# Optimization experiments

Measured on AMD Instinct MI355X. Metric: run time of the kernel, lower is better.

## Reference

```python
import jax, jax.numpy as jnp
import numpy as np

N_NODES = 100000
N_EDGES = 1600000
H = 64
TEM = 30.0
LN_EPS = 1e-5


def _mk_params(key):
    ks = jax.random.split(key, 6)
    s = 0.05
    p = {
        # edge_mlp: Linear(2H,H) relu Linear(H,H) relu (act_last=True)
        'We1': jax.random.normal(ks[0], (2 * H, H), jnp.float32) * s,
        'be1': jnp.zeros((H,), jnp.float32),
        'We2': jax.random.normal(ks[1], (H, H), jnp.float32) * s,
        'be2': jnp.zeros((H,), jnp.float32),
        # edge_inf: Linear(H,1)
        'Winf': jax.random.normal(ks[2], (H, 1), jnp.float32) * s,
        'binf': jnp.zeros((1,), jnp.float32),
        # node_mlp: Linear(2H,H) relu Linear(H,H) (no act_last)
        'Wn1': jax.random.normal(ks[3], (2 * H, H), jnp.float32) * s,
        'bn1': jnp.zeros((H,), jnp.float32),
        'Wn2': jax.random.normal(ks[4], (H, H), jnp.float32) * s,
        'bn2': jnp.zeros((H,), jnp.float32),
        # LayerNorm(H)
        'ln_g': jnp.ones((H,), jnp.float32),
        'ln_b': jnp.zeros((H,), jnp.float32),
    }
    return p


def setup_inputs() -> dict:
    key = jax.random.key(0)
    k1, k2, k3, k4 = jax.random.split(key, 4)
    inp = {
        'h': jax.random.normal(k1, (N_NODES, H), jnp.float32),
        'x': jax.random.normal(k2, (N_NODES, 3), jnp.float32),
        'edge_index': jax.random.randint(k3, (2, N_EDGES), 0, N_NODES, jnp.int64),
    }
    inp.update(_mk_params(k4))
    return inp


def _layernorm(z, g, b):
    mu = jnp.mean(z, axis=-1, keepdims=True)
    var = jnp.var(z, axis=-1, keepdims=True)
    return (z - mu) * jax.lax.rsqrt(var + LN_EPS) * g + b


def reference(h, x, edge_index, We1, be1, We2, be2, Winf, binf, Wn1, bn1, Wn2, bn2, ln_g, ln_b):
    src = edge_index[0]
    dst = edge_index[1]
    hi = h[dst]                      # [E, H]
    hj = h[src]                      # [E, H]
    rel_x = x[dst] - x[src]          # [E, 3]
    d_sq = jnp.sum(rel_x ** 2, axis=-1, keepdims=True)  # [E, 1]

    # edge MLP (relu, act_last=True)
    e_in = jnp.concatenate([hi, hj], axis=-1)           # [E, 2H]
    mij = jax.nn.relu(e_in @ We1 + be1)
    mij = jax.nn.relu(mij @ We2 + be2)                  # [E, H]

    eij = mij @ Winf + binf                             # [E, 1]
    edge_dis = jax.nn.sigmoid(TEM / (jnp.sqrt(d_sq) + 1e-8))
    edge_weights = jax.nn.sigmoid(eij * edge_dis)       # [E, 1]

    mi = jax.ops.segment_sum(mij * edge_weights, dst, num_segments=h.shape[0])  # [N, H]

    n_in = jnp.concatenate([mi, h], axis=-1)            # [N, 2H]
    upd = jax.nn.relu(n_in @ Wn1 + bn1) @ Wn2 + bn2     # [N, H] (no act_last)

    h_out = _layernorm(h + upd, ln_g, ln_b)
    return (h_out, x)
```

## Files before the change

### kernel.cpp

```cpp
#include <hip/hip_runtime.h>
#include <hip/hip_bf16.h>
#include <hip/hip_fp16.h>
#include <math.h>

#define HDIM 64
#define NN   100000
#define NE   1600000
#define TEMP 30.0f
#define LNEPS 1e-5f

#define GSH   6
#define GSZ   64
#define NB    1563
#define NBLK  64
#define EPB   (NE / NBLK)
#define NCNT  (NB * NBLK)
#define SCANB2 98
#define FSTR  72

typedef __attribute__((ext_vector_type(8))) short bf16x8;
typedef __attribute__((ext_vector_type(4))) float f32x4;
typedef _Float16 __attribute__((ext_vector_type(2))) h2t;

__device__ __forceinline__ short f2bf(float f) {
    __hip_bfloat16 b = __float2bfloat16(f);
    short s; __builtin_memcpy(&s, &b, 2); return s;
}
__device__ __forceinline__ unsigned pk2(float lo, float hi) {
    return (unsigned)(unsigned short)f2bf(lo) | ((unsigned)(unsigned short)f2bf(hi) << 16);
}
__device__ __forceinline__ short f2h(float f) {
    __half h = __float2half(f);
    short s; __builtin_memcpy(&s, &h, 2); return s;
}
__device__ __forceinline__ unsigned pk2h(float lo, float hi) {
    return (unsigned)(unsigned short)f2h(lo) | ((unsigned)(unsigned short)f2h(hi) << 16);
}
__device__ __forceinline__ unsigned pk_add_relu(unsigned a, unsigned b) {
    h2t x, y;
    __builtin_memcpy(&x, &a, 4); __builtin_memcpy(&y, &b, 4);
    h2t r = x + y;
    unsigned u; __builtin_memcpy(&u, &r, 4);
    const unsigned msk = ((u & 0x80008000u) >> 15) * 0xFFFFu;
    return u & ~msk;
}
__device__ __forceinline__ float sigmoidf_(float z) { return 1.0f / (1.0f + __expf(-z)); }

extern "C" __global__ void __launch_bounds__(256, 2)
front_kernel(const float* __restrict__ h,
             const float* __restrict__ We1, const float* __restrict__ be1,
             unsigned short* __restrict__ Pt, unsigned short* __restrict__ Pb,
             const int* __restrict__ ei, int* __restrict__ cnt3)
{
    __shared__ float fx[4][1024];
    const int b = blockIdx.x;

    if (b < NBLK) {
        int* hbin = (int*)&fx[0][0];
        const int tid = threadIdx.x;
        for (int k = tid; k < NB; k += 256) hbin[k] = 0;
        __syncthreads();
        const int i0 = b * EPB;
        for (int i = i0 + tid; i < i0 + EPB; i += 256)
            atomicAdd(&hbin[ei[NE + i] >> GSH], 1);
        __syncthreads();
        for (int k = tid; k < NB; k += 256)
            cnt3[k * NBLK + b] = hbin[k];
        return;
    }

    const int pb   = b - NBLK;
    const int tid  = threadIdx.x;
    const int wib  = tid >> 6;
    const int lane = tid & 63;
    const int e = lane & 15, g = lane >> 4;
    float* fb = &fx[wib][0];
    const int se = ((e & 1) << 4) | ((e >> 1) & 3);

    bf16x8 At[4][2], Ab[4][2];
    f32x4 b1r[4];
    #pragma unroll
    for (int t = 0; t < 4; ++t) {
        #pragma unroll
        for (int ks = 0; ks < 2; ++ks) {
            bf16x8 a, bb;
            #pragma unroll
            for (int j = 0; j < 8; ++j) {
                a[j]  = f2bf(We1[(32 * ks + 8 * g + j) * 64 + 16 * t + e]);
                bb[j] = f2bf(We1[(64 + 32 * ks + 8 * g + j) * 64 + 16 * t + e]);
            }
            At[t][ks] = a; Ab[t][ks] = bb;
        }
        #pragma unroll
        for (int r = 0; r < 4; ++r) b1r[t][r] = be1[16 * t + 4 * g + r];
    }

    const int gwid = pb * 4 + wib;
    const int nw   = 512 * 4;

    for (int tile = gwid; tile < NN / 16; tile += nw) {
        const int node = tile * 16 + e;

        bf16x8 B[2];
        #pragma unroll
        for (int ks = 0; ks < 2; ++ks) {
            const float4* p = (const float4*)(h + (size_t)node * 64 + ks * 32 + 8 * g);
            const float4 f0 = p[0], f1 = p[1];
            bf16x8 bb;
            bb[0] = f2bf(f0.x); bb[1] = f2bf(f0.y); bb[2] = f2bf(f0.z); bb[3] = f2bf(f0.w);
            bb[4] = f2bf(f1.x); bb[5] = f2bf(f1.y); bb[6] = f2bf(f1.z); bb[7] = f2bf(f1.w);
            B[ks] = bb;
        }

        f32x4 aT[4], aB[4];
        #pragma unroll
        for (int t = 0; t < 4; ++t) {
            aT[t] = b1r[t];
            aB[t] = (f32x4){0.f, 0.f, 0.f, 0.f};
            #pragma unroll
            for (int ks = 0; ks < 2; ++ks) {
                aT[t] = __builtin_amdgcn_mfma_f32_16x16x32_bf16(At[t][ks], B[ks], aT[t], 0, 0, 0);
                aB[t] = __builtin_amdgcn_mfma_f32_16x16x32_bf16(Ab[t][ks], B[ks], aB[t], 0, 0, 0);
            }
        }

        #pragma unroll
        for (int t = 0; t < 4; ++t)
            #pragma unroll
            for (int r = 0; r < 4; ++r)
                fb[e * 64 + ((16 * t + 4 * g + r) ^ se)] = aT[t][r];
        #pragma unroll
        for (int q = 0; q < 2; ++q) {
            const int row = q * 8 + (lane >> 3);
            const int sr  = ((row & 1) << 4) | ((row >> 1) & 3);
            const int c0  = (lane & 7) * 8;
            uint4 o;
            o.x = pk2h(fb[row * 64 + ((c0 + 0) ^ sr)], fb[row * 64 + ((c0 + 1) ^ sr)]);
            o.y = pk2h(fb[row * 64 + ((c0 + 2) ^ sr)], fb[row * 64 + ((c0 + 3) ^ sr)]);
            o.z = pk2h(fb[row * 64 + ((c0 + 4) ^ sr)], fb[row * 64 + ((c0 + 5) ^ sr)]);
            o.w = pk2h(fb[row * 64 + ((c0 + 6) ^ sr)], fb[row * 64 + ((c0 + 7) ^ sr)]);
            *(uint4*)((char*)Pt + (size_t)tile * 2048 + q * 1024 + lane * 16) = o;
        }

        #pragma unroll
        for (int t = 0; t < 4; ++t)
            #pragma unroll
            for (int r = 0; r < 4; ++r)
                fb[e * 64 + ((16 * t + 4 * g + r) ^ se)] = aB[t][r];
        #pragma unroll
        for (int q = 0; q < 2; ++q) {
            const int row = q * 8 + (lane >> 3);
            const int sr  = ((row & 1) << 4) | ((row >> 1) & 3);
            const int c0  = (lane & 7) * 8;
            uint4 o;
            o.x = pk2h(fb[row * 64 + ((c0 + 0) ^ sr)], fb[row * 64 + ((c0 + 1) ^ sr)]);
            o.y = pk2h(fb[row * 64 + ((c0 + 2) ^ sr)], fb[row * 64 + ((c0 + 3) ^ sr)]);
            o.z = pk2h(fb[row * 64 + ((c0 + 4) ^ sr)], fb[row * 64 + ((c0 + 5) ^ sr)]);
            o.w = pk2h(fb[row * 64 + ((c0 + 6) ^ sr)], fb[row * 64 + ((c0 + 7) ^ sr)]);
            *(uint4*)((char*)Pb + (size_t)tile * 2048 + q * 1024 + lane * 16) = o;
        }
    }
}

extern "C" __global__ void __launch_bounds__(1024)
scanA_kernel(const int* __restrict__ cnt3, int* __restrict__ off3, int* __restrict__ bsum)
{
    __shared__ int sh[1024];
    const int t = threadIdx.x;
    const int i = blockIdx.x * 1024 + t;
    const int v = (i < NCNT) ? cnt3[i] : 0;
    sh[t] = v;
    __syncthreads();
    for (int off = 1; off < 1024; off <<= 1) {
        const int u = (t >= off) ? sh[t - off] : 0;
        __syncthreads();
        sh[t] += u;
        __syncthreads();
    }
    if (i < NCNT) off3[i] = sh[t] - v;
    if (t == 1023) bsum[blockIdx.x] = sh[1023];
}

extern "C" __global__ void __launch_bounds__(128)
scanB_kernel(int* __restrict__ bsum)
{
    __shared__ int sh[128];
    const int t = threadIdx.x;
    const int v = (t < SCANB2) ? bsum[t] : 0;
    sh[t] = v;
    __syncthreads();
    for (int off = 1; off < 128; off <<= 1) {
        const int u = (t >= off) ? sh[t - off] : 0;
        __syncthreads();
        sh[t] += u;
        __syncthreads();
    }
    if (t < SCANB2) bsum[t] = sh[t] - v;
}

extern "C" __global__ void __launch_bounds__(1024)
scanC_kernel(int* __restrict__ off3, const int* __restrict__ bsum)
{
    const int i = blockIdx.x * 1024 + threadIdx.x;
    if (i < NCNT) off3[i] += bsum[blockIdx.x];
}

extern "C" __global__ void __launch_bounds__(1024)
scatter3_kernel(const int* __restrict__ ei, const int* __restrict__ off3,
                unsigned* __restrict__ sedge)
{
    __shared__ int cur[NB];
    const int b   = blockIdx.x;
    const int tid = threadIdx.x;
    for (int k = tid; k < NB; k += 1024) cur[k] = off3[k * NBLK + b];
    __syncthreads();
    const int i0 = b * EPB;
    for (int i = i0 + tid; i < i0 + EPB; i += 1024) {
        const int s = ei[i];
        const int d = ei[NE + i];
        const int pos = atomicAdd(&cur[d >> GSH], 1);
        sedge[pos] = (unsigned)s | ((unsigned)(d & (GSZ - 1)) << 17);
    }
}

extern "C" __global__ void __launch_bounds__(256)
sort2_kernel(const unsigned* __restrict__ sedge, const int* __restrict__ off3,
             int2* __restrict__ spair)
{
    __shared__ int hist[GSZ], base[GSZ], curs[GSZ];
    const int tid = threadIdx.x;
    const int b   = blockIdx.x;
    const int r0  = off3[b * NBLK];
    const int r1  = (b == NB - 1) ? NE : off3[(b + 1) * NBLK];

    if (tid < GSZ) hist[tid] = 0;
    __syncthreads();
    for (int i = r0 + tid; i < r1; i += 256)
        atomicAdd(&hist[(sedge[i] >> 17) & (GSZ - 1)], 1);
    __syncthreads();
    if (tid == 0) {
        int run = 0;
        for (int j = 0; j < GSZ; ++j) { base[j] = run; run += hist[j]; }
    }
    __syncthreads();
    if (tid < GSZ) curs[tid] = base[tid];
    __syncthreads();
    for (int i = r0 + tid; i < r1; i += 256) {
        const unsigned pk = sedge[i];
        const int dl = (pk >> 17) & (GSZ - 1);
        const int pos = r0 + atomicAdd(&curs[dl], 1);
        spair[pos] = make_int2((int)(pk & 0x1FFFFu), (b << GSH) | dl);
    }
}

extern "C" __global__ void __launch_bounds__(256, 2)
edge_kernel_sorted(const unsigned short* __restrict__ Pt, const unsigned short* __restrict__ Pb,
                   const float* __restrict__ x, const int2* __restrict__ spair,
                   const float* __restrict__ We2, const float* __restrict__ be2,
                   const float* __restrict__ Winf, const float* __restrict__ binf,
                   float* __restrict__ mi)
{
    __shared__ float fx[4][16 * FSTR];
    const int tid  = threadIdx.x;
    const int wib  = tid >> 6;
    const int lane = tid & 63;
    const int e = lane & 15, g = lane >> 4;
    float* fb = &fx[wib][0];

    bf16x8 A2[4][2];
    f32x4 b2r[4], wir[4];
    #pragma unroll
    for (int t = 0; t < 4; ++t) {
        #pragma unroll
        for (int ks = 0; ks < 2; ++ks) {
            bf16x8 a;
            #pragma unroll
            for (int j = 0; j < 8; ++j)
                a[j] = f2h(We2[(32 * ks + 8 * g + j) * 64 + 16 * t + e]);
            A2[t][ks] = a;
        }
        #pragma unroll
        for (int r = 0; r < 4; ++r) {
            b2r[t][r] = be2[16 * t + 4 * g + r];
            wir[t][r] = Winf[16 * t + 4 * g + r];
        }
    }
    const float binf0 = binf[0];

    const int NT     = NE / 16;
    const int nwaves = gridDim.x * 4;
    const int gwid   = blockIdx.x * 4 + wib;
    const int chunk  = (NT + nwaves - 1) / nwaves;
    const int t0 = gwid * chunk;
    const int t1 = (t0 + chunk < NT) ? t0 + chunk : NT;

    float racc  = 0.f;
    int   rrow  = -1;

    for (int tile = t0; tile < t1; ++tile) {
        const int eid = tile * 16 + e;
        const int2 sd = spair[eid];
        const int sN = sd.x;
        const int dN = sd.y;

        const float dx = x[dN * 3 + 0] - x[sN * 3 + 0];
        const float dy = x[dN * 3 + 1] - x[sN * 3 + 1];
        const float dz = x[dN * 3 + 2] - x[sN * 3 + 2];
        const float dsq = dx * dx + dy * dy + dz * dz;
        const float edis = sigmoidf_(TEMP / (sqrtf(dsq) + 1e-8f));

        bf16x8 B2[2];
        #pragma unroll
        for (int ks = 0; ks < 2; ++ks) {
            const uint4 ut = *(const uint4*)(Pt + (size_t)dN * 64 + 32 * ks + 8 * g);
            const uint4 ub = *(const uint4*)(Pb + (size_t)sN * 64 + 32 * ks + 8 * g);
            union { uint4 u; bf16x8 b; } cvt;
            cvt.u.x = pk_add_relu(ut.x, ub.x);
            cvt.u.y = pk_add_relu(ut.y, ub.y);
            cvt.u.z = pk_add_relu(ut.z, ub.z);
            cvt.u.w = pk_add_relu(ut.w, ub.w);
            B2[ks] = cvt.b;
        }

        f32x4 acc2[4];
        #pragma unroll
        for (int t = 0; t < 4; ++t) {
            acc2[t] = b2r[t];
            #pragma unroll
            for (int ks = 0; ks < 2; ++ks)
                acc2[t] = __builtin_amdgcn_mfma_f32_16x16x32_f16(A2[t][ks], B2[ks], acc2[t], 0, 0, 0);
        }

        float m[4][4];
        float p = 0.f;
        #pragma unroll
        for (int t = 0; t < 4; ++t)
            #pragma unroll
            for (int r = 0; r < 4; ++r) {
                m[t][r] = fmaxf(acc2[t][r], 0.f);
                p = fmaf(m[t][r], wir[t][r], p);
            }
        p += __shfl_xor(p, 16);
        p += __shfl_xor(p, 32);
        const float w = sigmoidf_((p + binf0) * edis);

        #pragma unroll
        for (int t = 0; t < 4; ++t) {
            float4 v;
            v.x = m[t][0] * w; v.y = m[t][1] * w;
            v.z = m[t][2] * w; v.w = m[t][3] * w;
            *(float4*)&fb[e * FSTR + 16 * t + 4 * g] = v;
        }

        #pragma unroll
        for (int i = 0; i < 16; ++i) {
            const int row = __builtin_amdgcn_readlane(dN, i);
            const float v = fb[i * FSTR + lane];
            if (row != rrow) {
                if (rrow >= 0) atomicAdd(mi + (size_t)rrow * 64 + lane, racc);
                rrow = row; racc = v;
            } else {
                racc += v;
            }
        }
    }
    if (rrow >= 0) atomicAdd(mi + (size_t)rrow * 64 + lane, racc);
}

extern "C" __global__ void __launch_bounds__(256, 2)
edge_kernel_unsorted(const unsigned short* __restrict__ Pt, const unsigned short* __restrict__ Pb,
                     const float* __restrict__ x, const int* __restrict__ ei,
                     const float* __restrict__ We2, const float* __restrict__ be2,
                     const float* __restrict__ Winf, const float* __restrict__ binf,
                     float* __restrict__ mi)
{
    __shared__ float fx[4][16 * FSTR];
    const int tid  = threadIdx.x;
    const int wib  = tid >> 6;
    const int lane = tid & 63;
    const int e = lane & 15, g = lane >> 4;
    float* fb = &fx[wib][0];

    bf16x8 A2[4][2];
    f32x4 b2r[4], wir[4];
    #pragma unroll
    for (int t = 0; t < 4; ++t) {
        #pragma unroll
        for (int ks = 0; ks < 2; ++ks) {
            bf16x8 a;
            #pragma unroll
            for (int j = 0; j < 8; ++j)
                a[j] = f2h(We2[(32 * ks + 8 * g + j) * 64 + 16 * t + e]);
            A2[t][ks] = a;
        }
        #pragma unroll
        for (int r = 0; r < 4; ++r) {
            b2r[t][r] = be2[16 * t + 4 * g + r];
            wir[t][r] = Winf[16 * t + 4 * g + r];
        }
    }
    const float binf0 = binf[0];

    const int gwid = blockIdx.x * 4 + wib;
    const int nw   = gridDim.x * 4;

    for (int tile = gwid; tile < NE / 16; tile += nw) {
        const int eid = tile * 16 + e;
        const int sN = ei[eid];
        const int dN = ei[NE + eid];

        const float dx = x[dN * 3 + 0] - x[sN * 3 + 0];
        const float dy = x[dN * 3 + 1] - x[sN * 3 + 1];
        const float dz = x[dN * 3 + 2] - x[sN * 3 + 2];
        const float dsq = dx * dx + dy * dy + dz * dz;
        const float edis = sigmoidf_(TEMP / (sqrtf(dsq) + 1e-8f));

        bf16x8 B2[2];
        #pragma unroll
        for (int ks = 0; ks < 2; ++ks) {
            const uint4 ut = *(const uint4*)(Pt + (size_t)dN * 64 + 32 * ks + 8 * g);
            const uint4 ub = *(const uint4*)(Pb + (size_t)sN * 64 + 32 * ks + 8 * g);
            union { uint4 u; bf16x8 b; } cvt;
            cvt.u.x = pk_add_relu(ut.x, ub.x);
            cvt.u.y = pk_add_relu(ut.y, ub.y);
            cvt.u.z = pk_add_relu(ut.z, ub.z);
            cvt.u.w = pk_add_relu(ut.w, ub.w);
            B2[ks] = cvt.b;
        }

        f32x4 acc2[4];
        #pragma unroll
        for (int t = 0; t < 4; ++t) {
            acc2[t] = b2r[t];
            #pragma unroll
            for (int ks = 0; ks < 2; ++ks)
                acc2[t] = __builtin_amdgcn_mfma_f32_16x16x32_f16(A2[t][ks], B2[ks], acc2[t], 0, 0, 0);
        }

        float m[4][4];
        float p = 0.f;
        #pragma unroll
        for (int t = 0; t < 4; ++t)
            #pragma unroll
            for (int r = 0; r < 4; ++r) {
                m[t][r] = fmaxf(acc2[t][r], 0.f);
                p = fmaf(m[t][r], wir[t][r], p);
            }
        p += __shfl_xor(p, 16);
        p += __shfl_xor(p, 32);
        const float w = sigmoidf_((p + binf0) * edis);

        #pragma unroll
        for (int t = 0; t < 4; ++t) {
            float4 v;
            v.x = m[t][0] * w; v.y = m[t][1] * w;
            v.z = m[t][2] * w; v.w = m[t][3] * w;
            *(float4*)&fb[e * FSTR + 16 * t + 4 * g] = v;
        }

        #pragma unroll
        for (int i = 0; i < 16; ++i) {
            const int row = __shfl(dN, i);
            const float v = fb[i * FSTR + lane];
            atomicAdd(mi + (size_t)row * 64 + lane, v);
        }
    }
}

extern "C" __global__ void __launch_bounds__(256, 2)
node_kernel(const float* __restrict__ h, const float* __restrict__ mi_,
            const float* __restrict__ Wn1, const float* __restrict__ bn1,
            const float* __restrict__ Wn2, const float* __restrict__ bn2,
            const float* __restrict__ lng, const float* __restrict__ lnb,
            float* __restrict__ out)
{
    __shared__ unsigned xlds[4][16 * 32];
    const int tid  = threadIdx.x;
    const int wib  = tid >> 6;
    const int lane = tid & 63;
    const int e = lane & 15, g = lane >> 4;
    unsigned* tb = &xlds[wib][0];
    const int sw = (e & 7) << 2;

    bf16x8 A1[4][4], A2[4][2];
    f32x4 b1r[4], b2r[4], gr[4], br[4];
    #pragma unroll
    for (int t = 0; t < 4; ++t) {
        #pragma unroll
        for (int ks = 0; ks < 4; ++ks) {
            bf16x8 a;
            #pragma unroll
            for (int j = 0; j < 8; ++j)
                a[j] = f2bf(Wn1[(32 * ks + 8 * g + j) * 64 + 16 * t + e]);
            A1[t][ks] = a;
        }
        #pragma unroll
        for (int ks = 0; ks < 2; ++ks) {
            bf16x8 a;
            #pragma unroll
            for (int j = 0; j < 8; ++j)
                a[j] = f2bf(Wn2[(32 * ks + 8 * g + j) * 64 + 16 * t + e]);
            A2[t][ks] = a;
        }
        #pragma unroll
        for (int r = 0; r < 4; ++r) {
            b1r[t][r] = bn1[16 * t + 4 * g + r];
            b2r[t][r] = bn2[16 * t + 4 * g + r];
            gr[t][r]  = lng[16 * t + 4 * g + r];
            br[t][r]  = lnb[16 * t + 4 * g + r];
        }
    }

    const int gwid = blockIdx.x * 4 + wib;
    const int nw   = gridDim.x * 4;

    for (int tile = gwid; tile < NN / 16; tile += nw) {
        const int node = tile * 16 + e;

        bf16x8 B1[4];
        #pragma unroll
        for (int ks = 0; ks < 4; ++ks) {
            const float* srcp = (ks < 2) ? mi_ : h;
            const float4* p = (const float4*)(srcp + (size_t)node * 64 + (ks & 1) * 32 + 8 * g);
            const float4 f0 = p[0], f1 = p[1];
            bf16x8 b;
            b[0] = f2bf(f0.x); b[1] = f2bf(f0.y); b[2] = f2bf(f0.z); b[3] = f2bf(f0.w);
            b[4] = f2bf(f1.x); b[5] = f2bf(f1.y); b[6] = f2bf(f1.z); b[7] = f2bf(f1.w);
            B1[ks] = b;
        }

        f32x4 acc1[4];
        #pragma unroll
        for (int t = 0; t < 4; ++t) {
            acc1[t] = b1r[t];
            #pragma unroll
            for (int ks = 0; ks < 4; ++ks)
                acc1[t] = __builtin_amdgcn_mfma_f32_16x16x32_bf16(A1[t][ks], B1[ks], acc1[t], 0, 0, 0);
        }

        #pragma unroll
        for (int t = 0; t < 4; ++t) {
            const float r0 = fmaxf(acc1[t][0], 0.f), r1 = fmaxf(acc1[t][1], 0.f);
            const float r2 = fmaxf(acc1[t][2], 0.f), r3 = fmaxf(acc1[t][3], 0.f);
            tb[e * 32 + ((8 * t + 2 * g + 0) ^ sw)] = pk2(r0, r1);
            tb[e * 32 + ((8 * t + 2 * g + 1) ^ sw)] = pk2(r2, r3);
        }
        bf16x8 B2[2];
        #pragma unroll
        for (int ks = 0; ks < 2; ++ks) {
            union { uint4 u; bf16x8 b; } cvt;
            cvt.u = *(const uint4*)&tb[e * 32 + ((16 * ks + 4 * g) ^ sw)];
            B2[ks] = cvt.b;
        }

        f32x4 acc2[4];
        #pragma unroll
        for (int t = 0; t < 4; ++t) {
            acc2[t] = b2r[t];
            #pragma unroll
            for (int ks = 0; ks < 2; ++ks)
                acc2[t] = __builtin_amdgcn_mfma_f32_16x16x32_bf16(A2[t][ks], B2[ks], acc2[t], 0, 0, 0);
        }

        float z[4][4];
        float s1 = 0.f, s2 = 0.f;
        #pragma unroll
        for (int t = 0; t < 4; ++t) {
            const float4 hres = *(const float4*)(h + (size_t)node * 64 + 16 * t + 4 * g);
            #pragma unroll
            for (int r = 0; r < 4; ++r) {
                z[t][r] = acc2[t][r] + hres[r];
                s1 += z[t][r];
                s2 = fmaf(z[t][r], z[t][r], s2);
            }
        }
        s1 += __shfl_xor(s1, 16); s1 += __shfl_xor(s1, 32);
        s2 += __shfl_xor(s2, 16); s2 += __shfl_xor(s2, 32);
        const float mu   = s1 * (1.0f / 64.0f);
        const float var  = s2 * (1.0f / 64.0f) - mu * mu;
        const float rstd = rsqrtf(var + LNEPS);

        #pragma unroll
        for (int t = 0; t < 4; ++t) {
            float4 o;
            #pragma unroll
            for (int r = 0; r < 4; ++r)
                o[r] = (z[t][r] - mu) * rstd * gr[t][r] + br[t][r];
            *(float4*)(out + (size_t)node * 64 + 16 * t + 4 * g) = o;
        }
    }
}

extern "C" void kernel_launch(void* const* d_in, const int* in_sizes, int n_in,
                              void* d_out, int out_size, void* d_ws, size_t ws_size,
                              hipStream_t stream)
{
    const float* h    = (const float*)d_in[0];
    const float* x    = (const float*)d_in[1];
    const int*   ei   = (const int*)d_in[2];
    const float* We1  = (const float*)d_in[3];
    const float* be1  = (const float*)d_in[4];
    const float* We2  = (const float*)d_in[5];
    const float* be2  = (const float*)d_in[6];
    const float* Winf = (const float*)d_in[7];
    const float* binf = (const float*)d_in[8];
    const float* Wn1  = (const float*)d_in[9];
    const float* bn1  = (const float*)d_in[10];
    const float* Wn2  = (const float*)d_in[11];
    const float* bn2  = (const float*)d_in[12];
    const float* lng  = (const float*)d_in[13];
    const float* lnb  = (const float*)d_in[14];
    float* out = (float*)d_out;

    const size_t mi_bytes = (size_t)NN * HDIM * sizeof(float);
    const size_t p_bytes  = (size_t)NN * HDIM * sizeof(unsigned short);
    const size_t sp_bytes = (size_t)NE * sizeof(int2);
    const size_t se_bytes = (size_t)NE * sizeof(unsigned);
    const size_t c3_bytes = (size_t)NCNT * sizeof(int);

    const size_t need_sorted = mi_bytes + 2 * p_bytes + sp_bytes;

    if (ws_size >= need_sorted &&
        mi_bytes >= se_bytes + 2 * c3_bytes + SCANB2 * sizeof(int)) {
        char* ws = (char*)d_ws;
        float*          mi    = (float*)ws;              ws += mi_bytes;
        unsigned short* Pt    = (unsigned short*)ws;     ws += p_bytes;
        unsigned short* Pb    = (unsigned short*)ws;     ws += p_bytes;
        int2*           spair = (int2*)ws;

        char* mis = (char*)mi;
        unsigned* sedge = (unsigned*)mis;
        int*      cnt3  = (int*)(mis + se_bytes);
        int*      off3  = (int*)(mis + se_bytes + c3_bytes);
        int*      bsum  = (int*)(mis + se_bytes + 2 * c3_bytes);

        hipMemcpyAsync(out + (size_t)NN * HDIM, x, (size_t)NN * 3 * sizeof(float),
                       hipMemcpyDeviceToDevice, stream);

        front_kernel<<<NBLK + 512, 256, 0, stream>>>(h, We1, be1, Pt, Pb, ei, cnt3);
        scanA_kernel<<<SCANB2, 1024, 0, stream>>>(cnt3, off3, bsum);
        scanB_kernel<<<1, 128, 0, stream>>>(bsum);
        scanC_kernel<<<SCANB2, 1024, 0, stream>>>(off3, bsum);
        scatter3_kernel<<<NBLK, 1024, 0, stream>>>(ei, off3, sedge);
        sort2_kernel<<<NB, 256, 0, stream>>>(sedge, off3, spair);
        hipMemsetAsync(mi, 0, mi_bytes, stream);
        edge_kernel_sorted<<<2048, 256, 0, stream>>>(Pt, Pb, x, spair, We2, be2, Winf, binf, mi);
        node_kernel<<<512, 256, 0, stream>>>(h, mi, Wn1, bn1, Wn2, bn2, lng, lnb, out);
    } else {
        float* mi;
        unsigned short* Pt;
        unsigned short* Pb;
        if (ws_size >= mi_bytes + 2 * p_bytes) {
            mi = (float*)d_ws;
            Pt = (unsigned short*)((char*)d_ws + mi_bytes);
            Pb = (unsigned short*)((char*)d_ws + mi_bytes + p_bytes);
        } else {
            mi = out;
            Pt = (unsigned short*)d_ws;
            Pb = (unsigned short*)((char*)d_ws + p_bytes);
        }

        hipMemsetAsync(mi, 0, mi_bytes, stream);
        hipMemcpyAsync(out + (size_t)NN * HDIM, x, (size_t)NN * 3 * sizeof(float),
                       hipMemcpyDeviceToDevice, stream);

        front_kernel<<<NBLK + 512, 256, 0, stream>>>(h, We1, be1, Pt, Pb, ei,
                                                     (int*)((char*)d_ws));
        edge_kernel_unsorted<<<2048, 256, 0, stream>>>(Pt, Pb, x, ei, We2, be2, Winf, binf, mi);
        node_kernel<<<512, 256, 0, stream>>>(h, mi, Wn1, bn1, Wn2, bn2, lng, lnb, out);
    }
}
```

Measured before the change: 192.0 us.

## Software-pipeline edge gathers, fuse mi zeroing into front kernel, drop scanB

```diff
diff --git a/kernel.cpp b/kernel.cpp
--- a/kernel.cpp
+++ b/kernel.cpp
@@ -17,6 +17,7 @@
 #define NCNT  (NB * NBLK)
 #define SCANB2 98
 #define FSTR  72
+#define ZBLK  1563
 
 typedef __attribute__((ext_vector_type(8))) short bf16x8;
 typedef __attribute__((ext_vector_type(4))) float f32x4;
@@ -50,10 +51,23 @@
 front_kernel(const float* __restrict__ h,
              const float* __restrict__ We1, const float* __restrict__ be1,
              unsigned short* __restrict__ Pt, unsigned short* __restrict__ Pb,
-             const int* __restrict__ ei, int* __restrict__ cnt3)
+             const int* __restrict__ ei, int* __restrict__ cnt3,
+             float* __restrict__ mi_zero)
 {
     __shared__ float fx[4][1024];
     const int b = blockIdx.x;
+
+    if (b >= NBLK + 512) {
+        const int zb = b - NBLK - 512;
+        const size_t base = (size_t)zb * 4096;
+        float4* dst = (float4*)(mi_zero + base);
+        const size_t total = (size_t)NN * 64;
+        #pragma unroll
+        for (int i = threadIdx.x; i < 1024; i += 256)
+            if (base + (size_t)i * 4 < total)
+                dst[i] = (float4){0.f, 0.f, 0.f, 0.f};
+        return;
+    }
 
     if (b < NBLK) {
         int* hbin = (int*)&fx[0][0];
@@ -181,28 +195,21 @@
     if (t == 1023) bsum[blockIdx.x] = sh[1023];
 }
 
-extern "C" __global__ void __launch_bounds__(128)
-scanB_kernel(int* __restrict__ bsum)
-{
-    __shared__ int sh[128];
-    const int t = threadIdx.x;
-    const int v = (t < SCANB2) ? bsum[t] : 0;
-    sh[t] = v;
-    __syncthreads();
-    for (int off = 1; off < 128; off <<= 1) {
-        const int u = (t >= off) ? sh[t - off] : 0;
-        __syncthreads();
-        sh[t] += u;
-        __syncthreads();
-    }
-    if (t < SCANB2) bsum[t] = sh[t] - v;
-}
-
 extern "C" __global__ void __launch_bounds__(1024)
 scanC_kernel(int* __restrict__ off3, const int* __restrict__ bsum)
 {
-    const int i = blockIdx.x * 1024 + threadIdx.x;
-    if (i < NCNT) off3[i] += bsum[blockIdx.x];
+    __shared__ int boff;
+    const int t = threadIdx.x;
+    if (t < 64) {
+        int v = 0;
+        for (int j = t; j < blockIdx.x; j += 64) v += bsum[j];
+        #pragma unroll
+        for (int off = 1; off < 64; off <<= 1) v += __shfl_xor(v, off);
+        if (t == 0) boff = v;
+    }
+    __syncthreads();
+    const int i = blockIdx.x * 1024 + t;
+    if (i < NCNT) off3[i] += boff;
 }
 
 extern "C" __global__ void __launch_bounds__(1024)
@@ -297,11 +304,26 @@
     float racc  = 0.f;
     int   rrow  = -1;
 
+    int2 sdA, sdB;
+    uint4 g0, g1, g2, g3;
+    if (t0 < t1) {
+        sdA = spair[t0 * 16 + e];
+        g0 = *(const uint4*)(Pt + (size_t)sdA.y * 64 + 8 * g);
+        g1 = *(const uint4*)(Pt + (size_t)sdA.y * 64 + 32 + 8 * g);
+        g2 = *(const uint4*)(Pb + (size_t)sdA.x * 64 + 8 * g);
+        g3 = *(const uint4*)(Pb + (size_t)sdA.x * 64 + 32 + 8 * g);
+        sdB = (t0 + 1 < t1) ? spair[(t0 + 1) * 16 + e] : sdA;
+    }
+
     for (int tile = t0; tile < t1; ++tile) {
-        const int eid = tile * 16 + e;
-        const int2 sd = spair[eid];
-        const int sN = sd.x;
-        const int dN = sd.y;
+        const int2 sdC = (tile + 2 < t1) ? spair[(tile + 2) * 16 + e] : sdB;
+        const uint4 n0 = *(const uint4*)(Pt + (size_t)sdB.y * 64 + 8 * g);
+        const uint4 n1 = *(const uint4*)(Pt + (size_t)sdB.y * 64 + 32 + 8 * g);
+        const uint4 n2 = *(const uint4*)(Pb + (size_t)sdB.x * 64 + 8 * g);
+        const uint4 n3 = *(const uint4*)(Pb + (size_t)sdB.x * 64 + 32 + 8 * g);
+
+        const int sN = sdA.x;
+        const int dN = sdA.y;
 
         const float dx = x[dN * 3 + 0] - x[sN * 3 + 0];
         const float dy = x[dN * 3 + 1] - x[sN * 3 + 1];
@@ -310,16 +332,17 @@
         const float edis = sigmoidf_(TEMP / (sqrtf(dsq) + 1e-8f));
 
         bf16x8 B2[2];
-        #pragma unroll
-        for (int ks = 0; ks < 2; ++ks) {
-            const uint4 ut = *(const uint4*)(Pt + (size_t)dN * 64 + 32 * ks + 8 * g);
-            const uint4 ub = *(const uint4*)(Pb + (size_t)sN * 64 + 32 * ks + 8 * g);
-            union { uint4 u; bf16x8 b; } cvt;
-            cvt.u.x = pk_add_relu(ut.x, ub.x);
-            cvt.u.y = pk_add_relu(ut.y, ub.y);
-            cvt.u.z = pk_add_relu(ut.z, ub.z);
-            cvt.u.w = pk_add_relu(ut.w, ub.w);
-            B2[ks] = cvt.b;
+        {
+            union { uint4 u; bf16x8 b; } c0, c1;
+            c0.u.x = pk_add_relu(g0.x, g2.x);
+            c0.u.y = pk_add_relu(g0.y, g2.y);
+            c0.u.z = pk_add_relu(g0.z, g2.z);
+            c0.u.w = pk_add_relu(g0.w, g2.w);
+            c1.u.x = pk_add_relu(g1.x, g3.x);
+            c1.u.y = pk_add_relu(g1.y, g3.y);
+            c1.u.z = pk_add_relu(g1.z, g3.z);
+            c1.u.w = pk_add_relu(g1.w, g3.w);
+            B2[0] = c0.b; B2[1] = c1.b;
         }
 
         f32x4 acc2[4];
@@ -354,7 +377,7 @@
 
         #pragma unroll
         for (int i = 0; i < 16; ++i) {
-            const int row = __builtin_amdgcn_readlane(dN, i);
+            const int row = __builtin_amdgcn_readlane(sdA.y, i);
             const float v = fb[i * FSTR + lane];
             if (row != rrow) {
                 if (rrow >= 0) atomicAdd(mi + (size_t)rrow * 64 + lane, racc);
@@ -363,6 +386,9 @@
                 racc += v;
             }
         }
+
+        sdA = sdB; sdB = sdC;
+        g0 = n0; g1 = n1; g2 = n2; g3 = n3;
     }
     if (rrow >= 0) atomicAdd(mi + (size_t)rrow * 64 + lane, racc);
 }
@@ -617,18 +643,20 @@
     const size_t sp_bytes = (size_t)NE * sizeof(int2);
     const size_t se_bytes = (size_t)NE * sizeof(unsigned);
     const size_t c3_bytes = (size_t)NCNT * sizeof(int);
-
-    const size_t need_sorted = mi_bytes + 2 * p_bytes + sp_bytes;
-
-    if (ws_size >= need_sorted &&
-        mi_bytes >= se_bytes + 2 * c3_bytes + SCANB2 * sizeof(int)) {
+    const size_t scratch  = se_bytes + 2 * c3_bytes + SCANB2 * sizeof(int);
+
+    const size_t need_base  = mi_bytes + 2 * p_bytes + sp_bytes;
+    const size_t need_noali = need_base + scratch;
+
+    if (ws_size >= need_base && mi_bytes >= scratch) {
         char* ws = (char*)d_ws;
         float*          mi    = (float*)ws;              ws += mi_bytes;
         unsigned short* Pt    = (unsigned short*)ws;     ws += p_bytes;
         unsigned short* Pb    = (unsigned short*)ws;     ws += p_bytes;
-        int2*           spair = (int2*)ws;
-
-        char* mis = (char*)mi;
+        int2*           spair = (int2*)ws;               ws += sp_bytes;
+
+        const bool noalias = (ws_size >= need_noali);
+        char* mis = noalias ? ws : (char*)mi;
         unsigned* sedge = (unsigned*)mis;
         int*      cnt3  = (int*)(mis + se_bytes);
         int*      off3  = (int*)(mis + se_bytes + c3_bytes);
@@ -637,13 +665,20 @@
         hipMemcpyAsync(out + (size_t)NN * HDIM, x, (size_t)NN * 3 * sizeof(float),
                        hipMemcpyDeviceToDevice, stream);
 
-        front_kernel<<<NBLK + 512, 256, 0, stream>>>(h, We1, be1, Pt, Pb, ei, cnt3);
-        scanA_kernel<<<SCANB2, 1024, 0, stream>>>(cnt3, off3, bsum);
-        scanB_kernel<<<1, 128, 0, stream>>>(bsum);
-        scanC_kernel<<<SCANB2, 1024, 0, stream>>>(off3, bsum);
-        scatter3_kernel<<<NBLK, 1024, 0, stream>>>(ei, off3, sedge);
-        sort2_kernel<<<NB, 256, 0, stream>>>(sedge, off3, spair);
-        hipMemsetAsync(mi, 0, mi_bytes, stream);
+        if (noalias) {
+            front_kernel<<<NBLK + 512 + ZBLK, 256, 0, stream>>>(h, We1, be1, Pt, Pb, ei, cnt3, mi);
+            scanA_kernel<<<SCANB2, 1024, 0, stream>>>(cnt3, off3, bsum);
+            scanC_kernel<<<SCANB2, 1024, 0, stream>>>(off3, bsum);
+            scatter3_kernel<<<NBLK, 1024, 0, stream>>>(ei, off3, sedge);
+            sort2_kernel<<<NB, 256, 0, stream>>>(sedge, off3, spair);
+        } else {
+            front_kernel<<<NBLK + 512, 256, 0, stream>>>(h, We1, be1, Pt, Pb, ei, cnt3, nullptr);
+            scanA_kernel<<<SCANB2, 1024, 0, stream>>>(cnt3, off3, bsum);
+            scanC_kernel<<<SCANB2, 1024, 0, stream>>>(off3, bsum);
+            scatter3_kernel<<<NBLK, 1024, 0, stream>>>(ei, off3, sedge);
+            sort2_kernel<<<NB, 256, 0, stream>>>(sedge, off3, spair);
+            hipMemsetAsync(mi, 0, mi_bytes, stream);
+        }
         edge_kernel_sorted<<<2048, 256, 0, stream>>>(Pt, Pb, x, spair, We2, be2, Winf, binf, mi);
         node_kernel<<<512, 256, 0, stream>>>(h, mi, Wn1, bn1, Wn2, bn2, lng, lnb, out);
     } else {
@@ -665,7 +700,7 @@
                        hipMemcpyDeviceToDevice, stream);
 
         front_kernel<<<NBLK + 512, 256, 0, stream>>>(h, We1, be1, Pt, Pb, ei,
-                                                     (int*)((char*)d_ws));
+                                                     (int*)((char*)d_ws), nullptr);
         edge_kernel_unsorted<<<2048, 256, 0, stream>>>(Pt, Pb, x, ei, We2, be2, Winf, binf, mi);
         node_kernel<<<512, 256, 0, stream>>>(h, mi, Wn1, bn1, Wn2, bn2, lng, lnb, out);
     }
```

Result: slower. 201.0 us (+4.7%).

## Fuse sort pass, node pre-projection and mi zeroing into one tail launch

Applied to the files above, without the earlier changes.

```diff
diff --git a/kernel.cpp b/kernel.cpp
--- a/kernel.cpp
+++ b/kernel.cpp
@@ -17,6 +17,7 @@
 #define NCNT  (NB * NBLK)
 #define SCANB2 98
 #define FSTR  72
+#define ZBLK  1563
 
 typedef __attribute__((ext_vector_type(8))) short bf16x8;
 typedef __attribute__((ext_vector_type(4))) float f32x4;
@@ -46,6 +47,148 @@
 }
 __device__ __forceinline__ float sigmoidf_(float z) { return 1.0f / (1.0f + __expf(-z)); }
 
+__device__ __forceinline__ void pre_body(int pb, int tid, float* fx4,
+                                         const float* __restrict__ h,
+                                         const float* __restrict__ We1,
+                                         const float* __restrict__ be1,
+                                         unsigned short* __restrict__ Pt,
+                                         unsigned short* __restrict__ Pb)
+{
+    const int wib  = tid >> 6;
+    const int lane = tid & 63;
+    const int e = lane & 15, g = lane >> 4;
+    float* fb = fx4 + wib * 1024;
+    const int se = ((e & 1) << 4) | ((e >> 1) & 3);
+
+    bf16x8 At[4][2], Ab[4][2];
+    f32x4 b1r[4];
+    #pragma unroll
+    for (int t = 0; t < 4; ++t) {
+        #pragma unroll
+        for (int ks = 0; ks < 2; ++ks) {
+            bf16x8 a, bb;
+            #pragma unroll
+            for (int j = 0; j < 8; ++j) {
+                a[j]  = f2bf(We1[(32 * ks + 8 * g + j) * 64 + 16 * t + e]);
+                bb[j] = f2bf(We1[(64 + 32 * ks + 8 * g + j) * 64 + 16 * t + e]);
+            }
+            At[t][ks] = a; Ab[t][ks] = bb;
+        }
+        #pragma unroll
+        for (int r = 0; r < 4; ++r) b1r[t][r] = be1[16 * t + 4 * g + r];
+    }
+
+    const int gwid = pb * 4 + wib;
+    const int nw   = 512 * 4;
+
+    for (int tile = gwid; tile < NN / 16; tile += nw) {
+        const int node = tile * 16 + e;
+
+        bf16x8 B[2];
+        #pragma unroll
+        for (int ks = 0; ks < 2; ++ks) {
+            const float4* p = (const float4*)(h + (size_t)node * 64 + ks * 32 + 8 * g);
+            const float4 f0 = p[0], f1 = p[1];
+            bf16x8 bb;
+            bb[0] = f2bf(f0.x); bb[1] = f2bf(f0.y); bb[2] = f2bf(f0.z); bb[3] = f2bf(f0.w);
+            bb[4] = f2bf(f1.x); bb[5] = f2bf(f1.y); bb[6] = f2bf(f1.z); bb[7] = f2bf(f1.w);
+            B[ks] = bb;
+        }
+
+        f32x4 aT[4], aB[4];
+        #pragma unroll
+        for (int t = 0; t < 4; ++t) {
+            aT[t] = b1r[t];
+            aB[t] = (f32x4){0.f, 0.f, 0.f, 0.f};
+            #pragma unroll
+            for (int ks = 0; ks < 2; ++ks) {
+                aT[t] = __builtin_amdgcn_mfma_f32_16x16x32_bf16(At[t][ks], B[ks], aT[t], 0, 0, 0);
+                aB[t] = __builtin_amdgcn_mfma_f32_16x16x32_bf16(Ab[t][ks], B[ks], aB[t], 0, 0, 0);
+            }
+        }
+
+        #pragma unroll
+        for (int t = 0; t < 4; ++t)
+            #pragma unroll
+            for (int r = 0; r < 4; ++r)
+                fb[e * 64 + ((16 * t + 4 * g + r) ^ se)] = aT[t][r];
+        #pragma unroll
+        for (int q = 0; q < 2; ++q) {
+            const int row = q * 8 + (lane >> 3);
+            const int sr  = ((row & 1) << 4) | ((row >> 1) & 3);
+            const int c0  = (lane & 7) * 8;
+            uint4 o;
+            o.x = pk2h(fb[row * 64 + ((c0 + 0) ^ sr)], fb[row * 64 + ((c0 + 1) ^ sr)]);
+            o.y = pk2h(fb[row * 64 + ((c0 + 2) ^ sr)], fb[row * 64 + ((c0 + 3) ^ sr)]);
+            o.z = pk2h(fb[row * 64 + ((c0 + 4) ^ sr)], fb[row * 64 + ((c0 + 5) ^ sr)]);
+            o.w = pk2h(fb[row * 64 + ((c0 + 6) ^ sr)], fb[row * 64 + ((c0 + 7) ^ sr)]);
+            *(uint4*)((char*)Pt + (size_t)tile * 2048 + q * 1024 + lane * 16) = o;
+        }
+
+        #pragma unroll
+        for (int t = 0; t < 4; ++t)
+            #pragma unroll
+            for (int r = 0; r < 4; ++r)
+                fb[e * 64 + ((16 * t + 4 * g + r) ^ se)] = aB[t][r];
+        #pragma unroll
+        for (int q = 0; q < 2; ++q) {
+            const int row = q * 8 + (lane >> 3);
+            const int sr  = ((row & 1) << 4) | ((row >> 1) & 3);
+            const int c0  = (lane & 7) * 8;
+            uint4 o;
+            o.x = pk2h(fb[row * 64 + ((c0 + 0) ^ sr)], fb[row * 64 + ((c0 + 1) ^ sr)]);
+            o.y = pk2h(fb[row * 64 + ((c0 + 2) ^ sr)], fb[row * 64 + ((c0 + 3) ^ sr)]);
+            o.z = pk2h(fb[row * 64 + ((c0 + 4) ^ sr)], fb[row * 64 + ((c0 + 5) ^ sr)]);
+            o.w = pk2h(fb[row * 64 + ((c0 + 6) ^ sr)], fb[row * 64 + ((c0 + 7) ^ sr)]);
+            *(uint4*)((char*)Pb + (size_t)tile * 2048 + q * 1024 + lane * 16) = o;
+        }
+    }
+}
+
+__device__ __forceinline__ void sort2_body(int b, int tid, int* hist, int* base, int* curs,
+                                           const unsigned* __restrict__ sedge,
+                                           const int* __restrict__ off3,
+                                           int2* __restrict__ spair)
+{
+    const int r0 = off3[b * NBLK];
+    const int r1 = (b == NB - 1) ? NE : off3[(b + 1) * NBLK];
+
+    if (tid < GSZ) hist[tid] = 0;
+    __syncthreads();
+    for (int i = r0 + tid; i < r1; i += 256)
+        atomicAdd(&hist[(sedge[i] >> 17) & (GSZ - 1)], 1);
+    __syncthreads();
+    if (tid == 0) {
+        int run = 0;
+        for (int j = 0; j < GSZ; ++j) { base[j] = run; run += hist[j]; }
+    }
+    __syncthreads();
+    if (tid < GSZ) curs[tid] = base[tid];
+    __syncthreads();
+    for (int i = r0 + tid; i < r1; i += 256) {
+        const unsigned pk = sedge[i];
+        const int dl = (pk >> 17) & (GSZ - 1);
+        const int pos = r0 + atomicAdd(&curs[dl], 1);
+        spair[pos] = make_int2((int)(pk & 0x1FFFFu), (b << GSH) | dl);
+    }
+}
+
+extern "C" __global__ void __launch_bounds__(256)
+hist_kernel(const int* __restrict__ ei, int* __restrict__ cnt3)
+{
+    __shared__ int hbin[NB];
+    const int b = blockIdx.x;
+    const int tid = threadIdx.x;
+    for (int k = tid; k < NB; k += 256) hbin[k] = 0;
+    __syncthreads();
+    const int i0 = b * EPB;
+    for (int i = i0 + tid; i < i0 + EPB; i += 256)
+        atomicAdd(&hbin[ei[NE + i] >> GSH], 1);
+    __syncthreads();
+    for (int k = tid; k < NB; k += 256)
+        cnt3[k * NBLK + b] = hbin[k];
+}
+
 extern "C" __global__ void __launch_bounds__(256, 2)
 front_kernel(const float* __restrict__ h,
              const float* __restrict__ We1, const float* __restrict__ be1,
@@ -54,7 +197,6 @@
 {
     __shared__ float fx[4][1024];
     const int b = blockIdx.x;
-
     if (b < NBLK) {
         int* hbin = (int*)&fx[0][0];
         const int tid = threadIdx.x;
@@ -68,98 +210,7 @@
             cnt3[k * NBLK + b] = hbin[k];
         return;
     }
-
-    const int pb   = b - NBLK;
-    const int tid  = threadIdx.x;
-    const int wib  = tid >> 6;
-    const int lane = tid & 63;
-    const int e = lane & 15, g = lane >> 4;
-    float* fb = &fx[wib][0];
-    const int se = ((e & 1) << 4) | ((e >> 1) & 3);
-
-    bf16x8 At[4][2], Ab[4][2];
-    f32x4 b1r[4];
-    #pragma unroll
-    for (int t = 0; t < 4; ++t) {
-        #pragma unroll
-        for (int ks = 0; ks < 2; ++ks) {
-            bf16x8 a, bb;
-            #pragma unroll
-            for (int j = 0; j < 8; ++j) {
-                a[j]  = f2bf(We1[(32 * ks + 8 * g + j) * 64 + 16 * t + e]);
-                bb[j] = f2bf(We1[(64 + 32 * ks + 8 * g + j) * 64 + 16 * t + e]);
-            }
-            At[t][ks] = a; Ab[t][ks] = bb;
-        }
-        #pragma unroll
-        for (int r = 0; r < 4; ++r) b1r[t][r] = be1[16 * t + 4 * g + r];
-    }
-
-    const int gwid = pb * 4 + wib;
-    const int nw   = 512 * 4;
-
-    for (int tile = gwid; tile < NN / 16; tile += nw) {
-        const int node = tile * 16 + e;
-
-        bf16x8 B[2];
-        #pragma unroll
-        for (int ks = 0; ks < 2; ++ks) {
-            const float4* p = (const float4*)(h + (size_t)node * 64 + ks * 32 + 8 * g);
-            const float4 f0 = p[0], f1 = p[1];
-            bf16x8 bb;
-            bb[0] = f2bf(f0.x); bb[1] = f2bf(f0.y); bb[2] = f2bf(f0.z); bb[3] = f2bf(f0.w);
-            bb[4] = f2bf(f1.x); bb[5] = f2bf(f1.y); bb[6] = f2bf(f1.z); bb[7] = f2bf(f1.w);
-            B[ks] = bb;
-        }
-
-        f32x4 aT[4], aB[4];
-        #pragma unroll
-        for (int t = 0; t < 4; ++t) {
-            aT[t] = b1r[t];
-            aB[t] = (f32x4){0.f, 0.f, 0.f, 0.f};
-            #pragma unroll
-            for (int ks = 0; ks < 2; ++ks) {
-                aT[t] = __builtin_amdgcn_mfma_f32_16x16x32_bf16(At[t][ks], B[ks], aT[t], 0, 0, 0);
-                aB[t] = __builtin_amdgcn_mfma_f32_16x16x32_bf16(Ab[t][ks], B[ks], aB[t], 0, 0, 0);
-            }
-        }
-
-        #pragma unroll
-        for (int t = 0; t < 4; ++t)
-            #pragma unroll
-            for (int r = 0; r < 4; ++r)
-                fb[e * 64 + ((16 * t + 4 * g + r) ^ se)] = aT[t][r];
-        #pragma unroll
-        for (int q = 0; q < 2; ++q) {
-            const int row = q * 8 + (lane >> 3);
-            const int sr  = ((row & 1) << 4) | ((row >> 1) & 3);
-            const int c0  = (lane & 7) * 8;
-            uint4 o;
-            o.x = pk2h(fb[row * 64 + ((c0 + 0) ^ sr)], fb[row * 64 + ((c0 + 1) ^ sr)]);
-            o.y = pk2h(fb[row * 64 + ((c0 + 2) ^ sr)], fb[row * 64 + ((c0 + 3) ^ sr)]);
-            o.z = pk2h(fb[row * 64 + ((c0 + 4) ^ sr)], fb[row * 64 + ((c0 + 5) ^ sr)]);
-            o.w = pk2h(fb[row * 64 + ((c0 + 6) ^ sr)], fb[row * 64 + ((c0 + 7) ^ sr)]);
-            *(uint4*)((char*)Pt + (size_t)tile * 2048 + q * 1024 + lane * 16) = o;
-        }
-
-        #pragma unroll
-        for (int t = 0; t < 4; ++t)
-            #pragma unroll
-            for (int r = 0; r < 4; ++r)
-                fb[e * 64 + ((16 * t + 4 * g + r) ^ se)] = aB[t][r];
-        #pragma unroll
-        for (int q = 0; q < 2; ++q) {
-            const int row = q * 8 + (lane >> 3);
-            const int sr  = ((row & 1) << 4) | ((row >> 1) & 3);
-            const int c0  = (lane & 7) * 8;
-            uint4 o;
-            o.x = pk2h(fb[row * 64 + ((c0 + 0) ^ sr)], fb[row * 64 + ((c0 + 1) ^ sr)]);
-            o.y = pk2h(fb[row * 64 + ((c0 + 2) ^ sr)], fb[row * 64 + ((c0 + 3) ^ sr)]);
-            o.z = pk2h(fb[row * 64 + ((c0 + 4) ^ sr)], fb[row * 64 + ((c0 + 5) ^ sr)]);
-            o.w = pk2h(fb[row * 64 + ((c0 + 6) ^ sr)], fb[row * 64 + ((c0 + 7) ^ sr)]);
-            *(uint4*)((char*)Pb + (size_t)tile * 2048 + q * 1024 + lane * 16) = o;
-        }
-    }
+    pre_body(b - NBLK, threadIdx.x, &fx[0][0], h, We1, be1, Pt, Pb);
 }
 
 extern "C" __global__ void __launch_bounds__(1024)
@@ -228,28 +279,36 @@
              int2* __restrict__ spair)
 {
     __shared__ int hist[GSZ], base[GSZ], curs[GSZ];
-    const int tid = threadIdx.x;
-    const int b   = blockIdx.x;
-    const int r0  = off3[b * NBLK];
-    const int r1  = (b == NB - 1) ? NE : off3[(b + 1) * NBLK];
-
-    if (tid < GSZ) hist[tid] = 0;
-    __syncthreads();
-    for (int i = r0 + tid; i < r1; i += 256)
-        atomicAdd(&hist[(sedge[i] >> 17) & (GSZ - 1)], 1);
-    __syncthreads();
-    if (tid == 0) {
-        int run = 0;
-        for (int j = 0; j < GSZ; ++j) { base[j] = run; run += hist[j]; }
-    }
-    __syncthreads();
-    if (tid < GSZ) curs[tid] = base[tid];
-    __syncthreads();
-    for (int i = r0 + tid; i < r1; i += 256) {
-        const unsigned pk = sedge[i];
-        const int dl = (pk >> 17) & (GSZ - 1);
-        const int pos = r0 + atomicAdd(&curs[dl], 1);
-        spair[pos] = make_int2((int)(pk & 0x1FFFFu), (b << GSH) | dl);
+    sort2_body(blockIdx.x, threadIdx.x, hist, base, curs, sedge, off3, spair);
+}
+
+extern "C" __global__ void __launch_bounds__(256, 2)
+tail_kernel(const unsigned* __restrict__ sedge, const int* __restrict__ off3,
+            int2* __restrict__ spair,
+            const float* __restrict__ h,
+            const float* __restrict__ We1, const float* __restrict__ be1,
+            unsigned short* __restrict__ Pt, unsigned short* __restrict__ Pb,
+            float* __restrict__ mi)
+{
+    __shared__ float fx[4][1024];
+    __shared__ int hist[GSZ], base[GSZ], curs[GSZ];
+    const int b = blockIdx.x;
+
+    if (b < NB) {
+        sort2_body(b, threadIdx.x, hist, base, curs, sedge, off3, spair);
+        return;
+    }
+    if (b < NB + 512) {
+        pre_body(b - NB, threadIdx.x, &fx[0][0], h, We1, be1, Pt, Pb);
+        return;
+    }
+    const int zb = b - NB - 512;
+    const size_t base4 = (size_t)zb * 1024;
+    const size_t tot4  = (size_t)NN * 16;
+    float4* dst = (float4*)mi;
+    for (int i = threadIdx.x; i < 1024; i += 256) {
+        const size_t idx = base4 + i;
+        if (idx < tot4) dst[idx] = (float4){0.f, 0.f, 0.f, 0.f};
     }
 }
 
@@ -617,18 +676,20 @@
     const size_t sp_bytes = (size_t)NE * sizeof(int2);
     const size_t se_bytes = (size_t)NE * sizeof(unsigned);
     const size_t c3_bytes = (size_t)NCNT * sizeof(int);
-
-    const size_t need_sorted = mi_bytes + 2 * p_bytes + sp_bytes;
-
-    if (ws_size >= need_sorted &&
-        mi_bytes >= se_bytes + 2 * c3_bytes + SCANB2 * sizeof(int)) {
+    const size_t scratch  = se_bytes + 2 * c3_bytes + SCANB2 * sizeof(int);
+
+    const size_t need_base  = mi_bytes + 2 * p_bytes + sp_bytes;
+    const size_t need_noali = need_base + scratch;
+
+    if (ws_size >= need_base && mi_bytes >= scratch) {
         char* ws = (char*)d_ws;
         float*          mi    = (float*)ws;              ws += mi_bytes;
         unsigned short* Pt    = (unsigned short*)ws;     ws += p_bytes;
         unsigned short* Pb    = (unsigned short*)ws;     ws += p_bytes;
-        int2*           spair = (int2*)ws;
-
-        char* mis = (char*)mi;
+        int2*           spair = (int2*)ws;               ws += sp_bytes;
+
+        const bool noalias = (ws_size >= need_noali);
+        char* mis = noalias ? ws : (char*)mi;
         unsigned* sedge = (unsigned*)mis;
         int*      cnt3  = (int*)(mis + se_bytes);
         int*      off3  = (int*)(mis + se_bytes + c3_bytes);
@@ -637,13 +698,23 @@
         hipMemcpyAsync(out + (size_t)NN * HDIM, x, (size_t)NN * 3 * sizeof(float),
                        hipMemcpyDeviceToDevice, stream);
 
-        front_kernel<<<NBLK + 512, 256, 0, stream>>>(h, We1, be1, Pt, Pb, ei, cnt3);
-        scanA_kernel<<<SCANB2, 1024, 0, stream>>>(cnt3, off3, bsum);
-        scanB_kernel<<<1, 128, 0, stream>>>(bsum);
-        scanC_kernel<<<SCANB2, 1024, 0, stream>>>(off3, bsum);
-        scatter3_kernel<<<NBLK, 1024, 0, stream>>>(ei, off3, sedge);
-        sort2_kernel<<<NB, 256, 0, stream>>>(sedge, off3, spair);
-        hipMemsetAsync(mi, 0, mi_bytes, stream);
+        if (noalias) {
+            hist_kernel<<<NBLK, 256, 0, stream>>>(ei, cnt3);
+            scanA_kernel<<<SCANB2, 1024, 0, stream>>>(cnt3, off3, bsum);
+            scanB_kernel<<<1, 128, 0, stream>>>(bsum);
+            scanC_kernel<<<SCANB2, 1024, 0, stream>>>(off3, bsum);
+            scatter3_kernel<<<NBLK, 1024, 0, stream>>>(ei, off3, sedge);
+            tail_kernel<<<NB + 512 + ZBLK, 256, 0, stream>>>(sedge, off3, spair,
+                                                             h, We1, be1, Pt, Pb, mi);
+        } else {
+            front_kernel<<<NBLK + 512, 256, 0, stream>>>(h, We1, be1, Pt, Pb, ei, cnt3);
+            scanA_kernel<<<SCANB2, 1024, 0, stream>>>(cnt3, off3, bsum);
+            scanB_kernel<<<1, 128, 0, stream>>>(bsum);
+            scanC_kernel<<<SCANB2, 1024, 0, stream>>>(off3, bsum);
+            scatter3_kernel<<<NBLK, 1024, 0, stream>>>(ei, off3, sedge);
+            sort2_kernel<<<NB, 256, 0, stream>>>(sedge, off3, spair);
+            hipMemsetAsync(mi, 0, mi_bytes, stream);
+        }
         edge_kernel_sorted<<<2048, 256, 0, stream>>>(Pt, Pb, x, spair, We2, be2, Winf, binf, mi);
         node_kernel<<<512, 256, 0, stream>>>(h, mi, Wn1, bn1, Wn2, bn2, lng, lnb, out);
     } else {
```

New measurement: 196.5 us. 2.4% more time.
